# Performance work log

Hardware: AMD Instinct MI355X
Metric: run time of the kernel (lower is better)

The kernel has to match this reference:

```python
import jax, jax.numpy as jnp
import numpy as np

S = 16384   # sequence length (tree derivation steps)
H = 512     # hidden size
E = 512     # action embedding size
R = 2048    # num_of_rules
L = 2       # GRU layers
PAD = -1    # learning_utils.PADDING_ACTION
OFF = 1     # learning_utils.UNIVERSAL_ACTION_OFFSET


def setup_inputs() -> dict:
    key = jax.random.key(0)
    ks = jax.random.split(key, 16)
    def n(k, shape, scale=0.05):
        return jax.random.normal(k, shape, jnp.float32) * scale
    emb = n(ks[1], (R + OFF, E)).at[PAD + OFF].set(0.0)  # padding_idx row zeroed
    return {
        "initial_state": n(ks[0], (L, 1, H)),
        "embedding": emb,
        "W_ih0": n(ks[2], (3 * H, 2 * E)),
        "W_hh0": n(ks[3], (3 * H, H)),
        "b_ih0": n(ks[4], (3 * H,)),
        "b_hh0": n(ks[5], (3 * H,)),
        "W_ih1": n(ks[6], (3 * H, H)),
        "W_hh1": n(ks[7], (3 * H, H)),
        "b_ih1": n(ks[8], (3 * H,)),
        "b_hh1": n(ks[9], (3 * H,)),
        "action_W": n(ks[10], (R, H)),
        "action_b": n(ks[11], (R,)),
        "value_W": n(ks[12], (1, H)),
        "value_b": n(ks[13], (1,)),
        "old_actions": jax.random.randint(ks[14], (S,), 0, R, jnp.int32),
        "old_parent_actions": jax.random.randint(ks[15], (S,), 0, R, jnp.int32),
    }


def gru_layer(x, h0, W_ih, W_hh, b_ih, b_hh):
    """Torch-semantics GRU over x:[S,In] with batch=1 squeezed; h0:[H]."""
    xi = x @ W_ih.T + b_ih  # precompute input gates [S, 3H]
    def step(h, xi_t):
        gh = h @ W_hh.T + b_hh
        xr, xz, xn = jnp.split(xi_t, 3)
        hr, hz, hn = jnp.split(gh, 3)
        r = jax.nn.sigmoid(xr + hr)
        z = jax.nn.sigmoid(xz + hz)
        nl = jnp.tanh(xn + r * hn)
        h_new = (1.0 - z) * nl + z * h
        return h_new, h_new
    _, out = jax.lax.scan(step, h0, xi)
    return out  # [S, H]


def reference(initial_state, embedding, W_ih0, W_hh0, b_ih0, b_hh0,
              W_ih1, W_hh1, b_ih1, b_hh1, action_W, action_b,
              value_W, value_b, old_actions, old_parent_actions):
    # teacher-forced shift: prepend PADDING_ACTION, drop last
    shifted = jnp.concatenate([jnp.array([PAD], old_actions.dtype), old_actions[:-1]])
    a_emb = embedding[shifted + OFF]             # [S, E]
    p_emb = embedding[old_parent_actions + OFF]  # [S, E]
    x = jnp.concatenate([a_emb, p_emb], axis=-1) # [S, 2E]
    h = gru_layer(x, initial_state[0, 0], W_ih0, W_hh0, b_ih0, b_hh0)
    out = gru_layer(h, initial_state[1, 0], W_ih1, W_hh1, b_ih1, b_hh1)
    log_probs = jax.nn.log_softmax(out @ action_W.T + action_b, axis=-1)  # [S, R]
    values = (out @ value_W.T + value_b)[:, 0]                            # [S]
    return log_probs, values
```

## Files before the change

### kernel.cpp

```cpp
#include <hip/hip_runtime.h>
#include <hip/hip_bf16.h>
#include <hip/hip_fp16.h>

typedef _Float16 f16;
typedef _Float16 f16x2 __attribute__((ext_vector_type(2)));
typedef _Float16 f16x4 __attribute__((ext_vector_type(4)));
typedef _Float16 f16x8 __attribute__((ext_vector_type(8)));
typedef float f32x4 __attribute__((ext_vector_type(4)));
typedef unsigned long long u64;

#define S_LEN 16384
#define NRULES 2048
#define CAP 2000000
#define FAST_TRIES 64

#define H1SEQ_OFF 0u
#define ACTW_OFF  (16u*1024*1024)
#define WIH0_OFF  (18u*1024*1024)
#define HB0F_OFF  (21u*1024*1024)
#define HB0S_OFF  (21u*1024*1024 + 4096)
#define HB1F_OFF  (21u*1024*1024 + 8192)
#define HB1S_OFF  (21u*1024*1024 + 12288)

#if __has_builtin(__builtin_amdgcn_rcpf)
#define RCPF(x) __builtin_amdgcn_rcpf(x)
#else
#define RCPF(x) (1.0f/(x))
#endif

union F2U { f16x2 f; unsigned u; };

__device__ __forceinline__ float sigf(float x){ return RCPF(1.0f + __expf(-x)); }
__device__ __forceinline__ float tanh_fast(float x){
  float ax = fabsf(x);
  float e = __expf(-2.0f*ax);
  float t = (1.0f - e) * RCPF(1.0f + e);
  return x >= 0.0f ? t : -t;
}
__device__ __forceinline__ float dot2(f16x2 a, f16x2 b, float c){
#if __has_builtin(__builtin_amdgcn_fdot2)
  return __builtin_amdgcn_fdot2(a, b, c, false);
#else
  return c + (float)a.x*(float)b.x + (float)a.y*(float)b.y;
#endif
}
__device__ __forceinline__ u64 aload64(const u64* p){
  return __hip_atomic_load(p, __ATOMIC_RELAXED, __HIP_MEMORY_SCOPE_AGENT);
}
__device__ __forceinline__ void apub64(u64* p, u64 v){
  (void)__hip_atomic_exchange(p, v, __ATOMIC_RELAXED, __HIP_MEMORY_SCOPE_AGENT);
}
__device__ __forceinline__ u64 load_sc0_u64(const u64* p){
  u64 v;
  asm volatile("global_load_dwordx2 %0, %1, off sc0\n\ts_waitcnt vmcnt(0)"
               : "=v"(v) : "v"(p) : "memory");
  return v;
}
__device__ __forceinline__ void store_u64(u64* p, u64 v){
  asm volatile("global_store_dwordx2 %0, %1, off"
               :: "v"(p), "v"(v) : "memory");
}

__global__ __launch_bounds__(256) void gather_x(
    const float* __restrict__ emb, const int* __restrict__ act,
    const int* __restrict__ par, f16* __restrict__ X)
{
  const int t = blockIdx.x, lid = threadIdx.x;
  const int ia = (t == 0) ? 0 : (act[t-1] + 1);
  const int ip = par[t] + 1;
  const int half = lid >> 7;
  const int k = (lid & 127) << 2;
  const float* src = emb + (size_t)(half ? ip : ia) * 512 + k;
  float4 v = *(const float4*)src;
  f16x4 o; o.x=(f16)v.x; o.y=(f16)v.y; o.z=(f16)v.z; o.w=(f16)v.w;
  *(f16x4*)&X[(size_t)t*1024 + (half<<9) + k] = o;
}

__global__ __launch_bounds__(256) void cvt_k(const float* __restrict__ in,
                                             f16* __restrict__ out, int n)
{
  const int i = (blockIdx.x*256 + threadIdx.x) << 2;
  if (i >= n) return;
  float4 v = *(const float4*)&in[i];
  f16x4 o; o.x=(f16)v.x; o.y=(f16)v.y; o.z=(f16)v.z; o.w=(f16)v.w;
  *(f16x4*)&out[i] = o;
}

__global__ __launch_bounds__(256) void init_ctrl(const float* __restrict__ init, char* ws)
{
  const int lid = threadIdx.x;
  u64* f0 = (u64*)(ws + HB0F_OFF);
  u64* s0 = (u64*)(ws + HB0S_OFF);
  u64* f1 = (u64*)(ws + HB1F_OFF);
  u64* s1 = (u64*)(ws + HB1S_OFF);
  F2U a; a.f.x=(f16)init[2*lid];     a.f.y=(f16)init[2*lid+1];
  F2U c; c.f.x=(f16)init[512+2*lid]; c.f.y=(f16)init[512+2*lid+1];
  const u64 inval = (u64)0xF0000000u << 32;
  const u64 sa = (u64)a.u, sc = (u64)c.u;
  f0[lid] = inval; f0[256+lid] = sa;
  s0[lid] = inval; s0[256+lid] = sa;
  f1[lid] = inval; f1[256+lid] = sc;
  s1[lid] = inval; s1[256+lid] = sc;
}

template<typename OutT>
__global__ __launch_bounds__(256) void gemm_f16(
    const f16* __restrict__ A, const f16* __restrict__ B,
    const float* __restrict__ bias, OutT* __restrict__ C,
    int M, int N, int K)
{
  __shared__ __align__(16) f16 At[4][128][8];
  __shared__ __align__(16) f16 Bt[4][128][8];
  const int lid = threadIdx.x;
  const int mtiles = M >> 7;
  const int bm = blockIdx.x % mtiles;
  const int bn = blockIdx.x / mtiles;
  const int m0 = bm << 7, n0 = bn << 7;
  const int lane = lid & 63, w = lid >> 6;
  const int wm = (w >> 1) << 6, wn = (w & 1) << 6;
  f32x4 acc[4][4] = {};
  const int nk = K >> 5;
  const int row1 = lid >> 2, j1 = lid & 3;
  for (int kt = 0; kt < nk; ++kt){
    const int kb = kt << 5;
    *(f16x8*)&At[j1][row1][0]    = *(const f16x8*)&A[(size_t)(m0+row1)*K    + kb + j1*8];
    *(f16x8*)&At[j1][row1+64][0] = *(const f16x8*)&A[(size_t)(m0+row1+64)*K + kb + j1*8];
    *(f16x8*)&Bt[j1][row1][0]    = *(const f16x8*)&B[(size_t)(n0+row1)*K    + kb + j1*8];
    *(f16x8*)&Bt[j1][row1+64][0] = *(const f16x8*)&B[(size_t)(n0+row1+64)*K + kb + j1*8];
    __syncthreads();
    const int kc = lane >> 4, rr = lane & 15;
    f16x8 aF[4], bF[4];
    #pragma unroll
    for (int m=0;m<4;m++) aF[m] = *(const f16x8*)&At[kc][wm + m*16 + rr][0];
    #pragma unroll
    for (int n=0;n<4;n++) bF[n] = *(const f16x8*)&Bt[kc][wn + n*16 + rr][0];
    #pragma unroll
    for (int m=0;m<4;m++)
      #pragma unroll
      for (int n=0;n<4;n++)
        acc[m][n] = __builtin_amdgcn_mfma_f32_16x16x32_f16(aF[m], bF[n], acc[m][n], 0,0,0);
    __syncthreads();
  }
  const int rr = lane & 15, rg = lane >> 4;
  #pragma unroll
  for (int n=0;n<4;n++){
    const int gcol = n0 + wn + n*16 + rr;
    const float bv = bias[gcol];
    #pragma unroll
    for (int m=0;m<4;m++){
      #pragma unroll
      for (int r=0;r<4;r++){
        const int grow = m0 + wm + m*16 + rg*4 + r;
        C[(size_t)grow*N + gcol] = (OutT)(acc[m][n][r] + bv);
      }
    }
  }
}

__global__ __launch_bounds__(256, 1) void scan_rings(
    const float* __restrict__ Whh0, const float* __restrict__ bhh0,
    const float* __restrict__ Wih1, const float* __restrict__ bih1,
    const float* __restrict__ Whh1, const float* __restrict__ bhh1,
    const float* __restrict__ init, const f16* __restrict__ xi0,
    u64* __restrict__ h0seq, char* ws)
{
  const int lid = threadIdx.x;
  const int bid = blockIdx.x;
  f16x2* h1seq = (f16x2*)(ws + H1SEQ_OFF);
  u64* hb0f = (u64*)(ws + HB0F_OFF);
  u64* hb0s = (u64*)(ws + HB0S_OFF);
  u64* hb1f = (u64*)(ws + HB1F_OFF);
  u64* hb1s = (u64*)(ws + HB1S_OFF);
  __shared__ f16x2 hx[256];
  __shared__ f16x2 hh[256];

  const int lane7 = bid & 7, grp = bid >> 3;
  bool fast_ok = true;

  if (lane7 == 0 && grp < 8){
    const int b = grp;
    const int ksub = lid & 3, row = (b << 6) + (lid >> 2);
    const bool owner = (ksub == 0);
    f16x2 wr[64], wz[64], wn[64];
    #pragma unroll
    for (int i=0;i<64;i++){
      const int k0 = (ksub + (i<<2)) << 1;
      float2 a = *(const float2*)&Whh0[(size_t)row*512         + k0];
      float2 bb= *(const float2*)&Whh0[(size_t)(512+row)*512   + k0];
      float2 c = *(const float2*)&Whh0[(size_t)(1024+row)*512  + k0];
      wr[i].x=(f16)a.x;  wr[i].y=(f16)a.y;
      wz[i].x=(f16)bb.x; wz[i].y=(f16)bb.y;
      wn[i].x=(f16)c.x;  wn[i].y=(f16)c.y;
    }
    float bhr=0.f, bhz=0.f, bhn=0.f;
    if (owner){ bhr=bhh0[row]; bhz=bhh0[512+row]; bhn=bhh0[1024+row]; }

    for (int q=0; q<S_LEN; ++q){
      float xr=0.f, xz=0.f, xn=0.f;
      if (owner){
        const f16* xp = xi0 + (size_t)q*1536;
        xr=(float)xp[row]; xz=(float)xp[512+row]; xn=(float)xp[1024+row];
      }
      {
        const int par = (q+1)&1;
        const u64* pf = hb0f + par*256 + lid;
        const u64* ps = hb0s + par*256 + lid;
        u64 cell = 0; bool got = false;
        if (fast_ok){
          for (int k=0;k<FAST_TRIES;k++){
            u64 v = load_sc0_u64(pf);
            if ((unsigned)(v>>32) == (unsigned)q){ cell=v; got=true; break; }
          }
          if (!got) fast_ok = false;
        }
        if (!got){
          int it=0;
          for(;;){ u64 v = aload64(ps);
                   if ((unsigned)(v>>32) == (unsigned)q){ cell=v; break; }
                   if (++it > CAP){ cell=v; break; } }
        }
        F2U cu; cu.u = (unsigned)cell; hx[lid] = cu.f;
      }
      __syncthreads();
      float ar=0.f, az=0.f, an=0.f;
      #pragma unroll
      for (int i=0;i<64;i++){
        f16x2 hv = hx[ksub + (i<<2)];
        ar = dot2(wr[i], hv, ar); az = dot2(wz[i], hv, az); an = dot2(wn[i], hv, an);
      }
      ar += __shfl_xor(ar,1); ar += __shfl_xor(ar,2);
      az += __shfl_xor(az,1); az += __shfl_xor(az,2);
      an += __shfl_xor(an,1); an += __shfl_xor(an,2);
      float hnew = 0.f;
      if (owner){
        float r  = sigf(xr + ar + bhr);
        float z  = sigf(xz + az + bhz);
        float nl = tanh_fast(xn + r*(an + bhn));
        hnew = (1.0f - z)*nl + z*(float)hx[row>>1][row&1];
      }
      float hp = __shfl(hnew, (lid & 192) + ((lid+4) & 63));
      if ((lid & 7) == 0){
        F2U pr; pr.f.x=(f16)hnew; pr.f.y=(f16)hp;
        const int j = (b<<5) + (lid>>3);
        const u64 tagged = ((u64)(unsigned)(q+1)<<32) | (u64)pr.u;
        store_u64(&hb0f[(q&1)*256 + j], tagged);
        apub64(&hb0s[(q&1)*256 + j], tagged);
        apub64(&h0seq[(size_t)q*256 + j], tagged);
      }
      __syncthreads();
    }
  } else if (lane7 == 1 && grp < 16){
    const int u = grp;
    const int ksub = lid & 7, row = (u << 5) + (lid >> 3);
    const bool owner = (ksub == 0);
    f16x2 ur[32], uz[32], un[32], vr[32], vz[32], vn[32];
    #pragma unroll
    for (int i=0;i<32;i++){
      const int k0 = (ksub + (i<<3)) << 1;
      float2 a = *(const float2*)&Wih1[(size_t)row*512        + k0];
      float2 bb= *(const float2*)&Wih1[(size_t)(512+row)*512  + k0];
      float2 c = *(const float2*)&Wih1[(size_t)(1024+row)*512 + k0];
      float2 d = *(const float2*)&Whh1[(size_t)row*512        + k0];
      float2 e = *(const float2*)&Whh1[(size_t)(512+row)*512  + k0];
      float2 f = *(const float2*)&Whh1[(size_t)(1024+row)*512 + k0];
      ur[i].x=(f16)a.x;  ur[i].y=(f16)a.y;
      uz[i].x=(f16)bb.x; uz[i].y=(f16)bb.y;
      un[i].x=(f16)c.x;  un[i].y=(f16)c.y;
      vr[i].x=(f16)d.x;  vr[i].y=(f16)d.y;
      vz[i].x=(f16)e.x;  vz[i].y=(f16)e.y;
      vn[i].x=(f16)f.x;  vn[i].y=(f16)f.y;
    }
    float bir=0.f,biz=0.f,bin=0.f, bhr=0.f,bhz=0.f,bhn=0.f;
    if (owner){
      bir=bih1[row]; biz=bih1[512+row]; bin=bih1[1024+row];
      bhr=bhh1[row]; bhz=bhh1[512+row]; bhn=bhh1[1024+row];
    }

    u64 ca_pref = 0;
    for (int t=0; t<S_LEN; ++t){
      const u64* pa = h0seq + (size_t)t*256 + lid;
      const int par = (t+1)&1;
      const u64* pf = hb1f + par*256 + lid;
      const u64* ps = hb1s + par*256 + lid;
      u64 ca=0, cb=0; bool ga=false, gb=false;
      if ((unsigned)(ca_pref>>32) == (unsigned)(t+1)){ ca=ca_pref; ga=true; }
      if (fast_ok){
        for (int k=0; k<FAST_TRIES && !(ga&&gb); ++k){
          if(!ga){ u64 v=aload64(pa);
                   if((unsigned)(v>>32)==(unsigned)(t+1)){ca=v;ga=true;} }
          if(!gb){ u64 v=load_sc0_u64(pf);
                   if((unsigned)(v>>32)==(unsigned)t){cb=v;gb=true;} }
        }
        if (!gb) fast_ok = false;
      }
      if (!(ga&&gb)){
        int it=0;
        while(!(ga&&gb)){
          if(!ga){ u64 v=aload64(pa);
                   if((unsigned)(v>>32)==(unsigned)(t+1)){ca=v;ga=true;} }
          if(!gb){ u64 v=aload64(ps);
                   if((unsigned)(v>>32)==(unsigned)t){cb=v;gb=true;} }
          if (++it > CAP) break;
        }
      }
      F2U xa; xa.u = (unsigned)ca; hx[lid] = xa.f;
      F2U hc; hc.u = (unsigned)cb; hh[lid] = hc.f;
      __syncthreads();
      if (t+1 < S_LEN) ca_pref = aload64(pa + 256);
      float ir=0.f, iz=0.f, in_=0.f, hr=0.f, hz=0.f, hn=0.f;
      #pragma unroll
      for (int i=0;i<32;i++){
        f16x2 xv = hx[ksub + (i<<3)];
        f16x2 hv = hh[ksub + (i<<3)];
        ir = dot2(ur[i], xv, ir); iz = dot2(uz[i], xv, iz); in_ = dot2(un[i], xv, in_);
        hr = dot2(vr[i], hv, hr); hz = dot2(vz[i], hv, hz); hn  = dot2(vn[i], hv, hn);
      }
      #pragma unroll
      for (int d=1; d<8; d<<=1){
        ir += __shfl_xor(ir,d); iz += __shfl_xor(iz,d); in_ += __shfl_xor(in_,d);
        hr += __shfl_xor(hr,d); hz += __shfl_xor(hz,d); hn  += __shfl_xor(hn,d);
      }
      float hnew = 0.f;
      if (owner){
        float r  = sigf(ir + bir + hr + bhr);
        float z  = sigf(iz + biz + hz + bhz);
        float nl = tanh_fast(in_ + bin + r*(hn + bhn));
        hnew = (1.0f - z)*nl + z*(float)hh[row>>1][row&1];
      }
      float hp = __shfl(hnew, (lid & 192) + ((lid+8) & 63));
      if ((lid & 15) == 0){
        F2U pr; pr.f.x=(f16)hnew; pr.f.y=(f16)hp;
        const int j = (u<<4) + (lid>>4);
        const u64 tagged = ((u64)(unsigned)(t+1)<<32) | (u64)pr.u;
        store_u64(&hb1f[(t&1)*256 + j], tagged);
        apub64(&hb1s[(t&1)*256 + j], tagged);
        h1seq[(size_t)t*256 + j] = pr.f;
      }
      __syncthreads();
    }
  }
}

__global__ __launch_bounds__(256) void logsoftmax_k(float* __restrict__ lp)
{
  const int t = blockIdx.x, lid = threadIdx.x;
  float* row = lp + (size_t)t*2048;
  float4 a = ((const float4*)row)[lid*2];
  float4 b = ((const float4*)row)[lid*2+1];
  float m = fmaxf(fmaxf(fmaxf(a.x,a.y),fmaxf(a.z,a.w)),
                  fmaxf(fmaxf(b.x,b.y),fmaxf(b.z,b.w)));
  #pragma unroll
  for (int off=1; off<64; off<<=1) m = fmaxf(m, __shfl_xor(m, off));
  __shared__ float redm[4], reds[4];
  const int lane = lid & 63, wvi = lid >> 6;
  if (lane==0) redm[wvi] = m;
  __syncthreads();
  m = fmaxf(fmaxf(redm[0],redm[1]), fmaxf(redm[2],redm[3]));
  float s = __expf(a.x-m)+__expf(a.y-m)+__expf(a.z-m)+__expf(a.w-m)
          + __expf(b.x-m)+__expf(b.y-m)+__expf(b.z-m)+__expf(b.w-m);
  #pragma unroll
  for (int off=1; off<64; off<<=1) s += __shfl_xor(s, off);
  if (lane==0) reds[wvi] = s;
  __syncthreads();
  s = reds[0]+reds[1]+reds[2]+reds[3];
  const float lg = m + __logf(s);
  a.x-=lg; a.y-=lg; a.z-=lg; a.w-=lg;
  b.x-=lg; b.y-=lg; b.z-=lg; b.w-=lg;
  ((float4*)row)[lid*2]   = a;
  ((float4*)row)[lid*2+1] = b;
}

__global__ __launch_bounds__(256) void values_k(
    const f16* __restrict__ h1, const float* __restrict__ vW,
    const float* __restrict__ vb, float* __restrict__ outv, int S)
{
  const int gt = (int)((blockIdx.x*256 + threadIdx.x) >> 6);
  if (gt >= S) return;
  const int lane = threadIdx.x & 63;
  const f16* rowp = h1 + (size_t)gt*512;
  float s = 0.f;
  #pragma unroll
  for (int j=0;j<8;j++){
    const int k = lane + (j<<6);
    s += (float)rowp[k] * vW[k];
  }
  #pragma unroll
  for (int off=32; off; off>>=1) s += __shfl_down(s, off);
  if (lane==0) outv[gt] = s + vb[0];
}

extern "C" void kernel_launch(void* const* d_in, const int* in_sizes, int n_in,
                              void* d_out, int out_size, void* d_ws, size_t ws_size,
                              hipStream_t stream) {
  const float* init = (const float*)d_in[0];
  const float* emb  = (const float*)d_in[1];
  const float* Wih0 = (const float*)d_in[2];
  const float* Whh0 = (const float*)d_in[3];
  const float* bih0 = (const float*)d_in[4];
  const float* bhh0 = (const float*)d_in[5];
  const float* Wih1 = (const float*)d_in[6];
  const float* Whh1 = (const float*)d_in[7];
  const float* bih1 = (const float*)d_in[8];
  const float* bhh1 = (const float*)d_in[9];
  const float* actW = (const float*)d_in[10];
  const float* actb = (const float*)d_in[11];
  const float* valW = (const float*)d_in[12];
  const float* valb = (const float*)d_in[13];
  const int*   acts = (const int*)d_in[14];
  const int*   pars = (const int*)d_in[15];
  float* out = (float*)d_out;
  char*  w   = (char*)d_ws;

  f16* h1seq = (f16*)(w + H1SEQ_OFF);
  f16* actWh = (f16*)(w + ACTW_OFF);
  f16* Wih0h = (f16*)(w + WIH0_OFF);
  f16* xi0   = (f16*)d_out;
  f16* X     = (f16*)((char*)d_out + 48u*1024*1024);
  u64* h0seq = (u64*)((char*)d_out + 80u*1024*1024);

  hipMemsetAsync(h0seq, 0, (size_t)S_LEN*256*8, stream);
  gather_x<<<S_LEN, 256, 0, stream>>>(emb, acts, pars, X);
  cvt_k<<<1536, 256, 0, stream>>>(Wih0, Wih0h, 1536*1024);
  cvt_k<<<1024, 256, 0, stream>>>(actW, actWh, 2048*512);
  init_ctrl<<<1, 256, 0, stream>>>(init, w);

  gemm_f16<f16><<<128*12, 256, 0, stream>>>(X, Wih0h, bih0, xi0, S_LEN, 1536, 1024);

  scan_rings<<<128, 256, 0, stream>>>(Whh0, bhh0, Wih1, bih1, Whh1, bhh1,
                                      init, xi0, h0seq, w);

  gemm_f16<float><<<128*16, 256, 0, stream>>>(h1seq, actWh, actb, out, S_LEN, NRULES, 512);
  logsoftmax_k<<<S_LEN, 256, 0, stream>>>(out);
  values_k<<<S_LEN/4, 256, 0, stream>>>(h1seq, valW, valb, out + (size_t)S_LEN*NRULES, S_LEN);
}
```

Measured before the change: 30.43 ms.

## Double-buffer scan state and poll next step's inputs after publishing

The persistent GRU scan kernel now seeds each block's shared state from the initial hidden state locally. The handshake is restructured so each step computes from a double-buffered shared copy, publishes, then polls for the next step's data. Layer 0 now also posts its per-step outputs to a fast (non-atomic) sequence buffer that layer 1 polls before falling back to the atomic buffer. Layer-1 blocks are moved to separate block IDs (grp 8..23) spread across the grid, the next xi0 row is loaded while waiting, and the spin cap becomes a shared budget. The aim is to cut cross-block latency on the serial critical path, at the cost of an extra memset and more complex polling that could misbehave if the fast loads see stale data.

```diff
diff --git a/kernel.cpp b/kernel.cpp
--- a/kernel.cpp
+++ b/kernel.cpp
@@ -11,8 +11,8 @@
 
 #define S_LEN 16384
 #define NRULES 2048
-#define CAP 2000000
 #define FAST_TRIES 64
+#define BUDGET 6000000
 
 #define H1SEQ_OFF 0u
 #define ACTW_OFF  (16u*1024*1024)
@@ -86,21 +86,18 @@
   *(f16x4*)&out[i] = o;
 }
 
-__global__ __launch_bounds__(256) void init_ctrl(const float* __restrict__ init, char* ws)
+__global__ __launch_bounds__(256) void init_ctrl(char* ws)
 {
   const int lid = threadIdx.x;
-  u64* f0 = (u64*)(ws + HB0F_OFF);
-  u64* s0 = (u64*)(ws + HB0S_OFF);
-  u64* f1 = (u64*)(ws + HB1F_OFF);
-  u64* s1 = (u64*)(ws + HB1S_OFF);
-  F2U a; a.f.x=(f16)init[2*lid];     a.f.y=(f16)init[2*lid+1];
-  F2U c; c.f.x=(f16)init[512+2*lid]; c.f.y=(f16)init[512+2*lid+1];
   const u64 inval = (u64)0xF0000000u << 32;
-  const u64 sa = (u64)a.u, sc = (u64)c.u;
-  f0[lid] = inval; f0[256+lid] = sa;
-  s0[lid] = inval; s0[256+lid] = sa;
-  f1[lid] = inval; f1[256+lid] = sc;
-  s1[lid] = inval; s1[256+lid] = sc;
+  u64* F0 = (u64*)(ws + HB0F_OFF);
+  u64* S0 = (u64*)(ws + HB0S_OFF);
+  u64* F1 = (u64*)(ws + HB1F_OFF);
+  u64* S1 = (u64*)(ws + HB1S_OFF);
+  F0[lid]=inval; F0[256+lid]=inval;
+  S0[lid]=inval; S0[256+lid]=inval;
+  F1[lid]=inval; F1[256+lid]=inval;
+  S1[lid]=inval; S1[256+lid]=inval;
 }
 
 template<typename OutT>
@@ -162,22 +159,23 @@
     const float* __restrict__ Wih1, const float* __restrict__ bih1,
     const float* __restrict__ Whh1, const float* __restrict__ bhh1,
     const float* __restrict__ init, const f16* __restrict__ xi0,
-    u64* __restrict__ h0seq, char* ws)
-{
-  const int lid = threadIdx.x;
-  const int bid = blockIdx.x;
+    u64* __restrict__ FST, u64* __restrict__ SST, char* ws)
+{
+  const int lid = threadIdx.x, bid = blockIdx.x;
+  if (bid & 7) return;
+  const int grp = bid >> 3;
+  if (grp >= 24) return;
   f16x2* h1seq = (f16x2*)(ws + H1SEQ_OFF);
-  u64* hb0f = (u64*)(ws + HB0F_OFF);
-  u64* hb0s = (u64*)(ws + HB0S_OFF);
-  u64* hb1f = (u64*)(ws + HB1F_OFF);
-  u64* hb1s = (u64*)(ws + HB1S_OFF);
-  __shared__ f16x2 hx[256];
-  __shared__ f16x2 hh[256];
-
-  const int lane7 = bid & 7, grp = bid >> 3;
+  u64* F0 = (u64*)(ws + HB0F_OFF);
+  u64* S0 = (u64*)(ws + HB0S_OFF);
+  u64* F1 = (u64*)(ws + HB1F_OFF);
+  u64* S1 = (u64*)(ws + HB1S_OFF);
+  __shared__ f16x2 hxA[2][256];
+  __shared__ f16x2 hxB[2][256];
   bool fast_ok = true;
-
-  if (lane7 == 0 && grp < 8){
+  int budget = BUDGET;
+
+  if (grp < 8){
     const int b = grp;
     const int ksub = lid & 3, row = (b << 6) + (lid >> 2);
     const bool owner = (ksub == 0);
@@ -192,65 +190,69 @@
       wz[i].x=(f16)bb.x; wz[i].y=(f16)bb.y;
       wn[i].x=(f16)c.x;  wn[i].y=(f16)c.y;
     }
-    float bhr=0.f, bhz=0.f, bhn=0.f;
-    if (owner){ bhr=bhh0[row]; bhz=bhh0[512+row]; bhn=bhh0[1024+row]; }
+    float bhr=0.f, bhz=0.f, bhn=0.f, xr=0.f, xz=0.f, xn=0.f;
+    if (owner){
+      bhr=bhh0[row]; bhz=bhh0[512+row]; bhn=bhh0[1024+row];
+      xr=(float)xi0[row]; xz=(float)xi0[512+row]; xn=(float)xi0[1024+row];
+    }
+    { F2U s; s.f.x=(f16)init[2*lid]; s.f.y=(f16)init[2*lid+1]; hxA[0][lid]=s.f; }
+    __syncthreads();
 
     for (int q=0; q<S_LEN; ++q){
-      float xr=0.f, xz=0.f, xn=0.f;
-      if (owner){
-        const f16* xp = xi0 + (size_t)q*1536;
-        xr=(float)xp[row]; xz=(float)xp[512+row]; xn=(float)xp[1024+row];
-      }
-      {
-        const int par = (q+1)&1;
-        const u64* pf = hb0f + par*256 + lid;
-        const u64* ps = hb0s + par*256 + lid;
-        u64 cell = 0; bool got = false;
-        if (fast_ok){
-          for (int k=0;k<FAST_TRIES;k++){
-            u64 v = load_sc0_u64(pf);
-            if ((unsigned)(v>>32) == (unsigned)q){ cell=v; got=true; break; }
-          }
-          if (!got) fast_ok = false;
-        }
-        if (!got){
-          int it=0;
-          for(;;){ u64 v = aload64(ps);
-                   if ((unsigned)(v>>32) == (unsigned)q){ cell=v; break; }
-                   if (++it > CAP){ cell=v; break; } }
-        }
-        F2U cu; cu.u = (unsigned)cell; hx[lid] = cu.f;
-      }
-      __syncthreads();
+      const int p = (q+1)&1;
+      const f16x2* cur = hxA[q&1];
       float ar=0.f, az=0.f, an=0.f;
       #pragma unroll
       for (int i=0;i<64;i++){
-        f16x2 hv = hx[ksub + (i<<2)];
-        ar = dot2(wr[i], hv, ar); az = dot2(wz[i], hv, az); an = dot2(wn[i], hv, an);
+        f16x2 hv = cur[ksub + (i<<2)];
+        ar = dot2(wr[i],hv,ar); az = dot2(wz[i],hv,az); an = dot2(wn[i],hv,an);
       }
       ar += __shfl_xor(ar,1); ar += __shfl_xor(ar,2);
       az += __shfl_xor(az,1); az += __shfl_xor(az,2);
       an += __shfl_xor(an,1); an += __shfl_xor(an,2);
       float hnew = 0.f;
       if (owner){
-        float r  = sigf(xr + ar + bhr);
-        float z  = sigf(xz + az + bhz);
-        float nl = tanh_fast(xn + r*(an + bhn));
-        hnew = (1.0f - z)*nl + z*(float)hx[row>>1][row&1];
+        float r_ = sigf(xr + ar + bhr);
+        float z_ = sigf(xz + az + bhz);
+        float nl = tanh_fast(xn + r_*(an + bhn));
+        hnew = (1.0f - z_)*nl + z_*(float)cur[row>>1][row&1];
       }
       float hp = __shfl(hnew, (lid & 192) + ((lid+4) & 63));
       if ((lid & 7) == 0){
         F2U pr; pr.f.x=(f16)hnew; pr.f.y=(f16)hp;
         const int j = (b<<5) + (lid>>3);
-        const u64 tagged = ((u64)(unsigned)(q+1)<<32) | (u64)pr.u;
-        store_u64(&hb0f[(q&1)*256 + j], tagged);
-        apub64(&hb0s[(q&1)*256 + j], tagged);
-        apub64(&h0seq[(size_t)q*256 + j], tagged);
+        const u64 tg = ((u64)(unsigned)(q+1)<<32) | (u64)pr.u;
+        store_u64(&F0[p*256 + j], tg);
+        store_u64(&FST[(size_t)q*256 + j], tg);
+        apub64(&S0[p*256 + j], tg);
+        apub64(&SST[(size_t)q*256 + j], tg);
+      }
+      if (owner && q+1 < S_LEN){
+        const f16* xp = xi0 + (size_t)(q+1)*1536;
+        xr=(float)xp[row]; xz=(float)xp[512+row]; xn=(float)xp[1024+row];
+      }
+      if (q+1 < S_LEN){
+        const u64* pf = F0 + p*256 + lid;
+        const u64* ps = S0 + p*256 + lid;
+        u64 cell=0; bool got=false;
+        if (fast_ok){
+          for (int k=0;k<FAST_TRIES;k++){
+            u64 v = load_sc0_u64(pf);
+            if ((unsigned)(v>>32) == (unsigned)(q+1)){ cell=v; got=true; break; }
+          }
+          if (!got) fast_ok = false;
+        }
+        if (!got){
+          for(;;){ u64 v = aload64(ps);
+                   if ((unsigned)(v>>32) == (unsigned)(q+1)){ cell=v; break; }
+                   if (--budget < 0){ cell=v; break; } }
+        }
+        F2U cu; cu.u = (unsigned)cell; hxA[p][lid] = cu.f;
       }
       __syncthreads();
     }
-  } else if (lane7 == 1 && grp < 16){
-    const int u = grp;
+  } else {
+    const int u = grp - 8;
     const int ksub = lid & 7, row = (u << 5) + (lid >> 3);
     const bool owner = (ksub == 0);
     f16x2 ur[32], uz[32], un[32], vr[32], vz[32], vn[32];
@@ -275,45 +277,33 @@
       bir=bih1[row]; biz=bih1[512+row]; bin=bih1[1024+row];
       bhr=bhh1[row]; bhz=bhh1[512+row]; bhn=bhh1[1024+row];
     }
-
-    u64 ca_pref = 0;
+    { F2U s; s.f.x=(f16)init[512+2*lid]; s.f.y=(f16)init[512+2*lid+1]; hxB[0][lid]=s.f; }
+    {
+      const u64* pf = FST + lid;
+      const u64* ps = SST + lid;
+      u64 cell=0;
+      for(;;){
+        u64 v = load_sc0_u64(pf);
+        if ((unsigned)(v>>32) == 1u){ cell=v; break; }
+        v = aload64(ps);
+        if ((unsigned)(v>>32) == 1u){ cell=v; break; }
+        if (--budget < 0){ cell=v; break; }
+      }
+      F2U cu; cu.u = (unsigned)cell; hxA[0][lid] = cu.f;
+    }
+    __syncthreads();
+
     for (int t=0; t<S_LEN; ++t){
-      const u64* pa = h0seq + (size_t)t*256 + lid;
-      const int par = (t+1)&1;
-      const u64* pf = hb1f + par*256 + lid;
-      const u64* ps = hb1s + par*256 + lid;
-      u64 ca=0, cb=0; bool ga=false, gb=false;
-      if ((unsigned)(ca_pref>>32) == (unsigned)(t+1)){ ca=ca_pref; ga=true; }
-      if (fast_ok){
-        for (int k=0; k<FAST_TRIES && !(ga&&gb); ++k){
-          if(!ga){ u64 v=aload64(pa);
-                   if((unsigned)(v>>32)==(unsigned)(t+1)){ca=v;ga=true;} }
-          if(!gb){ u64 v=load_sc0_u64(pf);
-                   if((unsigned)(v>>32)==(unsigned)t){cb=v;gb=true;} }
-        }
-        if (!gb) fast_ok = false;
-      }
-      if (!(ga&&gb)){
-        int it=0;
-        while(!(ga&&gb)){
-          if(!ga){ u64 v=aload64(pa);
-                   if((unsigned)(v>>32)==(unsigned)(t+1)){ca=v;ga=true;} }
-          if(!gb){ u64 v=aload64(ps);
-                   if((unsigned)(v>>32)==(unsigned)t){cb=v;gb=true;} }
-          if (++it > CAP) break;
-        }
-      }
-      F2U xa; xa.u = (unsigned)ca; hx[lid] = xa.f;
-      F2U hc; hc.u = (unsigned)cb; hh[lid] = hc.f;
-      __syncthreads();
-      if (t+1 < S_LEN) ca_pref = aload64(pa + 256);
+      const int p = (t+1)&1;
+      const f16x2* xcur = hxA[t&1];
+      const f16x2* hcur = hxB[t&1];
       float ir=0.f, iz=0.f, in_=0.f, hr=0.f, hz=0.f, hn=0.f;
       #pragma unroll
       for (int i=0;i<32;i++){
-        f16x2 xv = hx[ksub + (i<<3)];
-        f16x2 hv = hh[ksub + (i<<3)];
-        ir = dot2(ur[i], xv, ir); iz = dot2(uz[i], xv, iz); in_ = dot2(un[i], xv, in_);
-        hr = dot2(vr[i], hv, hr); hz = dot2(vz[i], hv, hz); hn  = dot2(vn[i], hv, hn);
+        f16x2 xv = xcur[ksub + (i<<3)];
+        f16x2 hv = hcur[ksub + (i<<3)];
+        ir = dot2(ur[i],xv,ir); iz = dot2(uz[i],xv,iz); in_ = dot2(un[i],xv,in_);
+        hr = dot2(vr[i],hv,hr); hz = dot2(vz[i],hv,hz); hn  = dot2(vn[i],hv,hn);
       }
       #pragma unroll
       for (int d=1; d<8; d<<=1){
@@ -322,19 +312,56 @@
       }
       float hnew = 0.f;
       if (owner){
-        float r  = sigf(ir + bir + hr + bhr);
-        float z  = sigf(iz + biz + hz + bhz);
-        float nl = tanh_fast(in_ + bin + r*(hn + bhn));
-        hnew = (1.0f - z)*nl + z*(float)hh[row>>1][row&1];
+        float r_ = sigf(ir + bir + hr + bhr);
+        float z_ = sigf(iz + biz + hz + bhz);
+        float nl = tanh_fast(in_ + bin + r_*(hn + bhn));
+        hnew = (1.0f - z_)*nl + z_*(float)hcur[row>>1][row&1];
       }
       float hp = __shfl(hnew, (lid & 192) + ((lid+8) & 63));
       if ((lid & 15) == 0){
         F2U pr; pr.f.x=(f16)hnew; pr.f.y=(f16)hp;
         const int j = (u<<4) + (lid>>4);
-        const u64 tagged = ((u64)(unsigned)(t+1)<<32) | (u64)pr.u;
-        store_u64(&hb1f[(t&1)*256 + j], tagged);
-        apub64(&hb1s[(t&1)*256 + j], tagged);
+        const u64 tg = ((u64)(unsigned)(t+1)<<32) | (u64)pr.u;
+        store_u64(&F1[p*256 + j], tg);
+        apub64(&S1[p*256 + j], tg);
         h1seq[(size_t)t*256 + j] = pr.f;
+      }
+      if (t+1 < S_LEN){
+        const u64* pfA = FST + (size_t)(t+1)*256 + lid;
+        const u64* psA = SST + (size_t)(t+1)*256 + lid;
+        const u64* pfB = F1 + p*256 + lid;
+        const u64* psB = S1 + p*256 + lid;
+        u64 ca=0, cb=0; bool ga=false, gb=false;
+        if (fast_ok){
+          for (int k=0; k<FAST_TRIES && !gb; ++k){
+            u64 v = load_sc0_u64(pfB);
+            if ((unsigned)(v>>32) == (unsigned)(t+1)){ cb=v; gb=true; }
+            if (!ga){
+              v = load_sc0_u64(pfA);
+              if ((unsigned)(v>>32) == (unsigned)(t+2)){ ca=v; ga=true; }
+            }
+          }
+          if (!gb) fast_ok = false;
+        }
+        while (!(ga && gb)){
+          if (!ga){
+            if (fast_ok){
+              u64 v = load_sc0_u64(pfA);
+              if ((unsigned)(v>>32) == (unsigned)(t+2)){ ca=v; ga=true; }
+            }
+            if (!ga){
+              u64 v = aload64(psA);
+              if ((unsigned)(v>>32) == (unsigned)(t+2)){ ca=v; ga=true; }
+            }
+          }
+          if (!gb){
+            u64 v = aload64(psB);
+            if ((unsigned)(v>>32) == (unsigned)(t+1)){ cb=v; gb=true; }
+          }
+          if (--budget < 0) break;
+        }
+        F2U xa; xa.u = (unsigned)ca; hxA[p][lid] = xa.f;
+        F2U hb; hb.u = (unsigned)cb; hxB[p][lid] = hb.f;
       }
       __syncthreads();
     }
@@ -414,20 +441,22 @@
   f16* h1seq = (f16*)(w + H1SEQ_OFF);
   f16* actWh = (f16*)(w + ACTW_OFF);
   f16* Wih0h = (f16*)(w + WIH0_OFF);
-  f16* xi0   = (f16*)d_out;
-  f16* X     = (f16*)((char*)d_out + 48u*1024*1024);
-  u64* h0seq = (u64*)((char*)d_out + 80u*1024*1024);
-
-  hipMemsetAsync(h0seq, 0, (size_t)S_LEN*256*8, stream);
+  f16* xi0 = (f16*)d_out;
+  f16* X   = (f16*)((char*)d_out + 48u*1024*1024);
+  u64* FST = (u64*)((char*)d_out + 48u*1024*1024);
+  u64* SST = (u64*)((char*)d_out + 80u*1024*1024);
+
   gather_x<<<S_LEN, 256, 0, stream>>>(emb, acts, pars, X);
   cvt_k<<<1536, 256, 0, stream>>>(Wih0, Wih0h, 1536*1024);
   cvt_k<<<1024, 256, 0, stream>>>(actW, actWh, 2048*512);
-  init_ctrl<<<1, 256, 0, stream>>>(init, w);
+  init_ctrl<<<1, 256, 0, stream>>>(w);
 
   gemm_f16<f16><<<128*12, 256, 0, stream>>>(X, Wih0h, bih0, xi0, S_LEN, 1536, 1024);
 
-  scan_rings<<<128, 256, 0, stream>>>(Whh0, bhh0, Wih1, bih1, Whh1, bhh1,
-                                      init, xi0, h0seq, w);
+  hipMemsetAsync(FST, 0, (size_t)S_LEN*256*8, stream);
+  hipMemsetAsync(SST, 0, (size_t)S_LEN*256*8, stream);
+  scan_rings<<<192, 256, 0, stream>>>(Whh0, bhh0, Wih1, bih1, Whh1, bhh1,
+                                      init, xi0, FST, SST, w);
 
   gemm_f16<float><<<128*16, 256, 0, stream>>>(h1seq, actWh, actb, out, S_LEN, NRULES, 512);
   logsoftmax_k<<<S_LEN, 256, 0, stream>>>(out);
```

Result: slower. 37.69 ms (+23.8%).

## Swizzle LDS hidden-state layout for 128-bit reads, double-buffer, prefetch gate inputs

Applied to the files above, without the earlier changes.

The hidden-state vector in LDS is stored with a swizzled slot mapping, so each k-subgroup reads its strided elements as contiguous f16x8 (128-bit) loads instead of many 32-bit LDS reads. The LDS buffers are double-buffered by step parity, and the barrier waits only on lgkmcnt. The next step's layer-0 input gates are loaded during the current step to take the xi0 global load off the recurrent critical path. The initial state is also written into the LDS buffer before the loop. The extra LDS buffer and the swizzle indexing add some complexity.

```diff
diff --git a/kernel.cpp b/kernel.cpp
--- a/kernel.cpp
+++ b/kernel.cpp
@@ -29,6 +29,10 @@
 #endif
 
 union F2U { f16x2 f; unsigned u; };
+union H8  { f16x8 v; f16x2 p[4]; };
+
+__device__ __forceinline__ int slot4(int j){ return ((j>>4)<<4) + ((j&3)<<2) + ((j>>2)&3); }
+__device__ __forceinline__ int slot8(int j){ return ((j>>5)<<5) + ((j&7)<<2) + ((j>>3)&3); }
 
 __device__ __forceinline__ float sigf(float x){ return RCPF(1.0f + __expf(-x)); }
 __device__ __forceinline__ float tanh_fast(float x){
@@ -60,6 +64,7 @@
   asm volatile("global_store_dwordx2 %0, %1, off"
                :: "v"(p), "v"(v) : "memory");
 }
+#define BAR_LGKM() asm volatile("s_waitcnt lgkmcnt(0)\n\ts_barrier" ::: "memory")
 
 __global__ __launch_bounds__(256) void gather_x(
     const float* __restrict__ emb, const int* __restrict__ act,
@@ -171,8 +176,8 @@
   u64* hb0s = (u64*)(ws + HB0S_OFF);
   u64* hb1f = (u64*)(ws + HB1F_OFF);
   u64* hb1s = (u64*)(ws + HB1S_OFF);
-  __shared__ f16x2 hx[256];
-  __shared__ f16x2 hh[256];
+  __shared__ __align__(16) f16x2 hx[2][256];
+  __shared__ __align__(16) f16x2 hh[2][256];
 
   const int lane7 = bid & 7, grp = bid >> 3;
   bool fast_ok = true;
@@ -192,17 +197,18 @@
       wz[i].x=(f16)bb.x; wz[i].y=(f16)bb.y;
       wn[i].x=(f16)c.x;  wn[i].y=(f16)c.y;
     }
-    float bhr=0.f, bhz=0.f, bhn=0.f;
-    if (owner){ bhr=bhh0[row]; bhz=bhh0[512+row]; bhn=bhh0[1024+row]; }
+    float bhr=0.f, bhz=0.f, bhn=0.f, xr=0.f, xz=0.f, xn=0.f;
+    if (owner){
+      bhr=bhh0[row]; bhz=bhh0[512+row]; bhn=bhh0[1024+row];
+      xr=(float)xi0[row]; xz=(float)xi0[512+row]; xn=(float)xi0[1024+row];
+    }
+    { F2U s; s.f.x=(f16)init[2*lid]; s.f.y=(f16)init[2*lid+1];
+      hx[0][slot4(lid)] = s.f; }
+    __syncthreads();
 
     for (int q=0; q<S_LEN; ++q){
-      float xr=0.f, xz=0.f, xn=0.f;
-      if (owner){
-        const f16* xp = xi0 + (size_t)q*1536;
-        xr=(float)xp[row]; xz=(float)xp[512+row]; xn=(float)xp[1024+row];
-      }
+      const int par = (q+1)&1;
       {
-        const int par = (q+1)&1;
         const u64* pf = hb0f + par*256 + lid;
         const u64* ps = hb0s + par*256 + lid;
         u64 cell = 0; bool got = false;
@@ -219,24 +225,36 @@
                    if ((unsigned)(v>>32) == (unsigned)q){ cell=v; break; }
                    if (++it > CAP){ cell=v; break; } }
         }
-        F2U cu; cu.u = (unsigned)cell; hx[lid] = cu.f;
-      }
-      __syncthreads();
+        F2U cu; cu.u = (unsigned)cell; hx[par][slot4(lid)] = cu.f;
+      }
+      float nxr=0.f, nxz=0.f, nxn=0.f;
+      if (owner && q+1 < S_LEN){
+        const f16* xp = xi0 + (size_t)(q+1)*1536;
+        nxr=(float)xp[row]; nxz=(float)xp[512+row]; nxn=(float)xp[1024+row];
+      }
+      BAR_LGKM();
+      const f16x2* hbase = &hx[par][ksub<<2];
       float ar=0.f, az=0.f, an=0.f;
       #pragma unroll
-      for (int i=0;i<64;i++){
-        f16x2 hv = hx[ksub + (i<<2)];
-        ar = dot2(wr[i], hv, ar); az = dot2(wz[i], hv, az); an = dot2(wn[i], hv, an);
+      for (int i4=0;i4<16;i4++){
+        H8 h; h.v = *(const f16x8*)(hbase + (i4<<4));
+        #pragma unroll
+        for (int m=0;m<4;m++){
+          const int i = (i4<<2)+m;
+          ar = dot2(wr[i],h.p[m],ar); az = dot2(wz[i],h.p[m],az); an = dot2(wn[i],h.p[m],an);
+        }
       }
       ar += __shfl_xor(ar,1); ar += __shfl_xor(ar,2);
       az += __shfl_xor(az,1); az += __shfl_xor(az,2);
       an += __shfl_xor(an,1); an += __shfl_xor(an,2);
       float hnew = 0.f;
       if (owner){
+        f16x2 pr2 = hx[par][slot4(row>>1)];
+        float h_old = (row&1) ? (float)pr2.y : (float)pr2.x;
         float r  = sigf(xr + ar + bhr);
         float z  = sigf(xz + az + bhz);
         float nl = tanh_fast(xn + r*(an + bhn));
-        hnew = (1.0f - z)*nl + z*(float)hx[row>>1][row&1];
+        hnew = (1.0f - z)*nl + z*h_old;
       }
       float hp = __shfl(hnew, (lid & 192) + ((lid+4) & 63));
       if ((lid & 7) == 0){
@@ -247,6 +265,7 @@
         apub64(&hb0s[(q&1)*256 + j], tagged);
         apub64(&h0seq[(size_t)q*256 + j], tagged);
       }
+      if (owner){ xr=nxr; xz=nxz; xn=nxn; }
       __syncthreads();
     }
   } else if (lane7 == 1 && grp < 16){
@@ -275,45 +294,56 @@
       bir=bih1[row]; biz=bih1[512+row]; bin=bih1[1024+row];
       bhr=bhh1[row]; bhz=bhh1[512+row]; bhn=bhh1[1024+row];
     }
+    { F2U s; s.f.x=(f16)init[512+2*lid]; s.f.y=(f16)init[512+2*lid+1];
+      hh[0][slot8(lid)] = s.f; }
+    __syncthreads();
 
     u64 ca_pref = 0;
     for (int t=0; t<S_LEN; ++t){
-      const u64* pa = h0seq + (size_t)t*256 + lid;
       const int par = (t+1)&1;
-      const u64* pf = hb1f + par*256 + lid;
-      const u64* ps = hb1s + par*256 + lid;
-      u64 ca=0, cb=0; bool ga=false, gb=false;
-      if ((unsigned)(ca_pref>>32) == (unsigned)(t+1)){ ca=ca_pref; ga=true; }
-      if (fast_ok){
-        for (int k=0; k<FAST_TRIES && !(ga&&gb); ++k){
-          if(!ga){ u64 v=aload64(pa);
-                   if((unsigned)(v>>32)==(unsigned)(t+1)){ca=v;ga=true;} }
-          if(!gb){ u64 v=load_sc0_u64(pf);
-                   if((unsigned)(v>>32)==(unsigned)t){cb=v;gb=true;} }
-        }
-        if (!gb) fast_ok = false;
-      }
-      if (!(ga&&gb)){
-        int it=0;
-        while(!(ga&&gb)){
-          if(!ga){ u64 v=aload64(pa);
-                   if((unsigned)(v>>32)==(unsigned)(t+1)){ca=v;ga=true;} }
-          if(!gb){ u64 v=aload64(ps);
-                   if((unsigned)(v>>32)==(unsigned)t){cb=v;gb=true;} }
-          if (++it > CAP) break;
-        }
-      }
-      F2U xa; xa.u = (unsigned)ca; hx[lid] = xa.f;
-      F2U hc; hc.u = (unsigned)cb; hh[lid] = hc.f;
-      __syncthreads();
-      if (t+1 < S_LEN) ca_pref = aload64(pa + 256);
+      {
+        const u64* pa = h0seq + (size_t)t*256 + lid;
+        const u64* pf = hb1f + par*256 + lid;
+        const u64* ps = hb1s + par*256 + lid;
+        u64 ca=0, cb=0; bool ga=false, gb=false;
+        if ((unsigned)(ca_pref>>32) == (unsigned)(t+1)){ ca=ca_pref; ga=true; }
+        if (fast_ok){
+          for (int k=0; k<FAST_TRIES && !(ga&&gb); ++k){
+            if(!ga){ u64 v=aload64(pa);
+                     if((unsigned)(v>>32)==(unsigned)(t+1)){ca=v;ga=true;} }
+            if(!gb){ u64 v=load_sc0_u64(pf);
+                     if((unsigned)(v>>32)==(unsigned)t){cb=v;gb=true;} }
+          }
+          if (!gb) fast_ok = false;
+        }
+        if (!(ga&&gb)){
+          int it=0;
+          while(!(ga&&gb)){
+            if(!ga){ u64 v=aload64(pa);
+                     if((unsigned)(v>>32)==(unsigned)(t+1)){ca=v;ga=true;} }
+            if(!gb){ u64 v=aload64(ps);
+                     if((unsigned)(v>>32)==(unsigned)t){cb=v;gb=true;} }
+            if (++it > CAP) break;
+          }
+        }
+        F2U xa; xa.u = (unsigned)ca; hx[par][slot8(lid)] = xa.f;
+        F2U hc; hc.u = (unsigned)cb; hh[par][slot8(lid)] = hc.f;
+      }
+      BAR_LGKM();
+      if (t+1 < S_LEN) ca_pref = aload64(h0seq + (size_t)(t+1)*256 + lid);
+      const f16x2* xbase = &hx[par][ksub<<2];
+      const f16x2* hbase = &hh[par][ksub<<2];
       float ir=0.f, iz=0.f, in_=0.f, hr=0.f, hz=0.f, hn=0.f;
       #pragma unroll
-      for (int i=0;i<32;i++){
-        f16x2 xv = hx[ksub + (i<<3)];
-        f16x2 hv = hh[ksub + (i<<3)];
-        ir = dot2(ur[i], xv, ir); iz = dot2(uz[i], xv, iz); in_ = dot2(un[i], xv, in_);
-        hr = dot2(vr[i], hv, hr); hz = dot2(vz[i], hv, hz); hn  = dot2(vn[i], hv, hn);
+      for (int i4=0;i4<8;i4++){
+        H8 xv; xv.v = *(const f16x8*)(xbase + (i4<<5));
+        H8 hv; hv.v = *(const f16x8*)(hbase + (i4<<5));
+        #pragma unroll
+        for (int m=0;m<4;m++){
+          const int i = (i4<<2)+m;
+          ir = dot2(ur[i],xv.p[m],ir); iz = dot2(uz[i],xv.p[m],iz); in_ = dot2(un[i],xv.p[m],in_);
+          hr = dot2(vr[i],hv.p[m],hr); hz = dot2(vz[i],hv.p[m],hz); hn  = dot2(vn[i],hv.p[m],hn);
+        }
       }
       #pragma unroll
       for (int d=1; d<8; d<<=1){
@@ -322,10 +352,12 @@
       }
       float hnew = 0.f;
       if (owner){
+        f16x2 pr2 = hh[par][slot8(row>>1)];
+        float h_old = (row&1) ? (float)pr2.y : (float)pr2.x;
         float r  = sigf(ir + bir + hr + bhr);
         float z  = sigf(iz + biz + hz + bhz);
         float nl = tanh_fast(in_ + bin + r*(hn + bhn));
-        hnew = (1.0f - z)*nl + z*(float)hh[row>>1][row&1];
+        hnew = (1.0f - z)*nl + z*h_old;
       }
       float hp = __shfl(hnew, (lid & 192) + ((lid+8) & 63));
       if ((lid & 15) == 0){
```

Result: no change. 29.85 ms (median of 2 runs) (-1.9%).
